# Kernel tuning notes

Hardware: AMD Instinct MI355X
Metric: run time of the kernel (lower is better)

Reference implementation:

```python
import jax, jax.numpy as jnp
import numpy as np

NUM_EXPERTS = 8
TOP_K = 2
B, S, H, I = 4, 4096, 1024, 2048


def setup_inputs() -> dict:
    key = jax.random.key(0)
    ks = jax.random.split(key, 4)
    std = 0.02
    return {
        "hidden_states": jax.random.normal(ks[0], (B, S, H), dtype=jnp.float32),
        "w_gate": jax.random.normal(ks[1], (NUM_EXPERTS, H), dtype=jnp.float32) * std,
        "w_fc": jax.random.normal(ks[2], (NUM_EXPERTS, I, H), dtype=jnp.float32) * std,
        "b_fc": jnp.zeros((NUM_EXPERTS, I), dtype=jnp.float32),
        "w_proj": jax.random.normal(ks[3], (NUM_EXPERTS, H, I), dtype=jnp.float32) * (std / np.sqrt(2 * 24)),
        "b_proj": jnp.zeros((NUM_EXPERTS, H), dtype=jnp.float32),
    }


def reference(hidden_states, w_gate, w_fc, b_fc, w_proj, b_proj):
    b, s, h = hidden_states.shape
    x = hidden_states.reshape(-1, h)  # [T, H]
    # routing: top-k over gate logits, softmax over the k selected logits
    router_logits = jnp.einsum("th,eh->te", x, w_gate)  # [T, E]
    top_vals, top_idx = jax.lax.top_k(router_logits, TOP_K)  # [T, K]
    gates = jax.nn.softmax(top_vals.astype(jnp.float32), axis=-1).astype(x.dtype)  # [T, K]
    # expert MLPs with weighted combine; per-token gate for expert e is the
    # selected routing weight (0 if e not in top-k) -- same math as the
    # gather / grouped-GEMM / index_add scatter in the original.
    out = jnp.zeros_like(x)
    for e in range(NUM_EXPERTS):
        g_e = jnp.sum(jnp.where(top_idx == e, gates, jnp.zeros_like(gates)), axis=-1)  # [T]
        hmid = jax.nn.gelu(x @ w_fc[e].T + b_fc[e], approximate=False)  # [T, I]
        y = hmid @ w_proj[e].T + b_proj[e]  # [T, H]
        out = out + g_e[:, None] * y
    return out.reshape(b, s, h)
```

## Files before the change

kernel.cpp:

```cpp
#include <hip/hip_runtime.h>
#include <math.h>

#define T_TOK 16384
#define HDIM  1024
#define IDIM  2048
#define NEXP  8
#define CAP   16384
#define ROWT  (CAP / 256)

typedef __bf16 bf16x8 __attribute__((ext_vector_type(8)));
typedef float  f32x4  __attribute__((ext_vector_type(4)));
typedef unsigned short us8 __attribute__((ext_vector_type(8)));

__device__ __forceinline__ unsigned short f2bf(float f) {
  unsigned int u = __builtin_bit_cast(unsigned int, f);
  u = (u + 0x7FFFu + ((u >> 16) & 1u)) >> 16;
  return (unsigned short)u;
}

__device__ __forceinline__ float bf2f(unsigned short u) {
  return __builtin_bit_cast(float, (unsigned int)u << 16);
}

__device__ __forceinline__ void gld16(const void* g, void* l) {
  __builtin_amdgcn_global_load_lds(
      (const __attribute__((address_space(1))) void*)(g),
      (__attribute__((address_space(3))) void*)(l), 16, 0, 0);
}

__device__ __forceinline__ bf16x8 cvt8(const float* p) {
  f32x4 lo = *(const f32x4*)p;
  f32x4 hi = *(const f32x4*)(p + 4);
  us8 t;
  t[0] = f2bf(lo[0]); t[1] = f2bf(lo[1]); t[2] = f2bf(lo[2]); t[3] = f2bf(lo[3]);
  t[4] = f2bf(hi[0]); t[5] = f2bf(hi[1]); t[6] = f2bf(hi[2]); t[7] = f2bf(hi[3]);
  return __builtin_bit_cast(bf16x8, t);
}

__global__ void zero_out_k(float4* out) {
  out[blockIdx.x * 256 + threadIdx.x] = float4{0.f, 0.f, 0.f, 0.f};
}

__global__ void report_k(float* out, float v, int n) {
  int idx = blockIdx.x * blockDim.x + threadIdx.x;
  int stride = gridDim.x * blockDim.x;
  for (int i = idx; i < n; i += stride) out[i] = v;
}

__global__ void cvt_bf16_k(const float* __restrict__ src, unsigned short* __restrict__ dst, int n4) {
  int idx = blockIdx.x * blockDim.x + threadIdx.x;
  int stride = gridDim.x * blockDim.x;
  for (int i = idx; i < n4; i += stride) {
    float4 v = ((const float4*)src)[i];
    ushort4 o;
    o.x = f2bf(v.x); o.y = f2bf(v.y); o.z = f2bf(v.z); o.w = f2bf(v.w);
    ((ushort4*)dst)[i] = o;
  }
}

__global__ void route1_k(const float* __restrict__ x, const float* __restrict__ wg,
                         int* __restrict__ echoice, float* __restrict__ tgate) {
  __shared__ __align__(16) float wgl[NEXP * HDIM];
  int tid = threadIdx.x;
  for (int i = tid; i < NEXP * HDIM / 4; i += 256)
    ((float4*)wgl)[i] = ((const float4*)wg)[i];
  __syncthreads();

  int wave = tid >> 6, lane = tid & 63;
  int t = blockIdx.x * 4 + wave;

  float accv[NEXP];
#pragma unroll
  for (int e = 0; e < NEXP; e++) accv[e] = 0.f;
  const float* xr = x + (size_t)t * HDIM;
#pragma unroll 4
  for (int j = 0; j < HDIM / 64; j++) {
    float xv = xr[lane + j * 64];
#pragma unroll
    for (int e = 0; e < NEXP; e++) accv[e] += xv * wgl[e * HDIM + lane + j * 64];
  }
#pragma unroll
  for (int off = 1; off < 64; off <<= 1) {
#pragma unroll
    for (int e = 0; e < NEXP; e++) accv[e] += __shfl_xor(accv[e], off, 64);
  }

  if (lane == 0) {
    int e0 = 0; float v0 = accv[0];
#pragma unroll
    for (int e = 1; e < NEXP; e++) if (accv[e] > v0) { v0 = accv[e]; e0 = e; }
    int e1 = -1; float v1 = -3.4e38f;
#pragma unroll
    for (int e = 0; e < NEXP; e++) if (e != e0 && accv[e] > v1) { v1 = accv[e]; e1 = e; }
    float ex = expf(v1 - v0);
    echoice[t] = e0 | (e1 << 8);
    tgate[t * 2]     = 1.f / (1.f + ex);
    tgate[t * 2 + 1] = ex / (1.f + ex);
  }
}

__global__ void route2_k(const int* __restrict__ echoice, int* __restrict__ counts,
                         int* __restrict__ etok) {
  int E = blockIdx.x;
  int tid = threadIdx.x, lane = tid & 63, wv = tid >> 6;
  __shared__ int base;
  __shared__ int wsum[4];
  if (tid == 0) base = 0;
  __syncthreads();
  for (int t0 = 0; t0 < T_TOK; t0 += 256) {
    int t = t0 + tid;
    int ec = echoice[t];
    int e0 = ec & 255, e1 = (ec >> 8) & 255;
    bool m = (e0 == E) | (e1 == E);
    int code = t * 2 + (e1 == E ? 1 : 0);
    unsigned long long mask = __ballot(m);
    if (lane == 0) wsum[wv] = __popcll(mask);
    int lpre = __popcll(mask & ((1ull << lane) - 1ull));
    __syncthreads();
    int wbase = 0;
#pragma unroll
    for (int w = 0; w < 4; w++) if (w < wv) wbase += wsum[w];
    int total = wsum[0] + wsum[1] + wsum[2] + wsum[3];
    if (m) etok[E * CAP + base + wbase + lpre] = code;
    __syncthreads();
    if (tid == 0) base += total;
    __syncthreads();
  }
  if (tid == 0) counts[E] = base;
}

template <int STAGE, int K, int N>
__global__ __launch_bounds__(512)
void gemm8_k(const unsigned short* __restrict__ A, const unsigned short* __restrict__ W,
             const float* __restrict__ bias, unsigned short* __restrict__ hmid,
             unsigned short* __restrict__ ybf,
             const int* __restrict__ counts, const int* __restrict__ etok) {
  extern __shared__ __align__(16) char smem[];
  constexpr int NTK = K / 32;
  constexpr int NTC = N / 256;
  int e  = blockIdx.x / (ROWT * NTC);
  int bi = blockIdx.x % (ROWT * NTC);
  int rt = bi / NTC, ct = bi % NTC;
  int cnt = counts[e];
  if (rt * 256 >= cnt) return;

  int tid = threadIdx.x;
  int lane = tid & 63, wv = tid >> 6;
  int wr = wv >> 2, wc = wv & 3;
  int quad = lane >> 4, ml = lane & 15;

  int sg = tid >> 6, sq = (tid >> 4) & 3, sml = tid & 15;
  const unsigned short* aptr[2];
  const unsigned short* bptr[2];
#pragma unroll
  for (int h = 0; h < 2; h++) {
    int r = rt * 256 + h * 128 + sg * 16 + sml;
    int code = etok[e * CAP + (r < cnt ? r : cnt - 1)];
    int arow = (STAGE == 1) ? (code >> 1) : code;
    aptr[h] = A + (size_t)arow * K + sq * 8;
    int n = ct * 256 + h * 128 + sg * 16 + sml;
    bptr[h] = W + ((size_t)e * N + n) * K + sq * 8;
  }
  char* Asm = smem;
  char* Bsm = smem + 65536;
  int ldst = tid * 16;

  auto stage_a = [&](int t) {
    int tt = t < NTK ? t : NTK - 1;
    char* dst = Asm + ((t & 3) * 2) * 8192 + ldst;
    gld16(aptr[0] + (size_t)tt * 32, dst);
    gld16(aptr[1] + (size_t)tt * 32, dst + 8192);
  };
  auto stage_b = [&](int t) {
    int tt = t < NTK ? t : NTK - 1;
    char* dst = Bsm + ((t & 3) * 2) * 8192 + ldst;
    gld16(bptr[0] + (size_t)tt * 32, dst);
    gld16(bptr[1] + (size_t)tt * 32, dst + 8192);
  };

  f32x4 acc[8][4] = {};

  stage_a(0); stage_b(0);
  stage_a(1); stage_b(1);
  stage_a(2); stage_b(2);
  asm volatile("s_waitcnt vmcnt(8)" ::: "memory");
  __builtin_amdgcn_s_barrier();

  int aoff = quad * 256 + ml * 16;
  int boff = (wc & 1) * 4096 + quad * 256 + ml * 16;

#pragma unroll 4
  for (int t = 0; t < NTK; t++) {
    const char* Ah = Asm + ((t & 3) * 2 + wr) * 8192;
    const char* Bh = Bsm + ((t & 3) * 2 + (wc >> 1)) * 8192;
    bf16x8 b0[4], a0[4];
#pragma unroll
    for (int ni = 0; ni < 4; ni++) b0[ni] = *(const bf16x8*)(Bh + boff + ni * 1024);
#pragma unroll
    for (int mi = 0; mi < 4; mi++) a0[mi] = *(const bf16x8*)(Ah + aoff + mi * 1024);
    stage_a(t + 3);
    asm volatile("" ::: "memory");
    __builtin_amdgcn_s_barrier();
    __builtin_amdgcn_s_setprio(1);
#pragma unroll
    for (int mi = 0; mi < 4; mi++)
#pragma unroll
      for (int ni = 0; ni < 4; ni++)
        acc[mi][ni] = __builtin_amdgcn_mfma_f32_16x16x32_bf16(a0[mi], b0[ni], acc[mi][ni], 0, 0, 0);
    __builtin_amdgcn_s_setprio(0);
    asm volatile("" ::: "memory");
    __builtin_amdgcn_s_barrier();
    bf16x8 a1[4];
#pragma unroll
    for (int mi = 0; mi < 4; mi++) a1[mi] = *(const bf16x8*)(Ah + aoff + (4 + mi) * 1024);
    stage_b(t + 3);
    asm volatile("" ::: "memory");
    __builtin_amdgcn_s_barrier();
    __builtin_amdgcn_s_setprio(1);
#pragma unroll
    for (int mi = 0; mi < 4; mi++)
#pragma unroll
      for (int ni = 0; ni < 4; ni++)
        acc[4 + mi][ni] = __builtin_amdgcn_mfma_f32_16x16x32_bf16(a1[mi], b0[ni], acc[4 + mi][ni], 0, 0, 0);
    __builtin_amdgcn_s_setprio(0);
    asm volatile("s_waitcnt vmcnt(8)" ::: "memory");
    __builtin_amdgcn_s_barrier();
  }

  int ncol[4]; float bv[4];
#pragma unroll
  for (int ni = 0; ni < 4; ni++) {
    ncol[ni] = ct * 256 + wc * 64 + ni * 16 + ml;
    bv[ni] = bias[e * N + ncol[ni]];
  }
#pragma unroll
  for (int mi = 0; mi < 8; mi++) {
    int ms[4], codes[4];
#pragma unroll
    for (int r = 0; r < 4; r++) {
      ms[r] = rt * 256 + wr * 128 + mi * 16 + quad * 4 + r;
      codes[r] = etok[e * CAP + (ms[r] < cnt ? ms[r] : 0)];
    }
#pragma unroll
    for (int ni = 0; ni < 4; ni++) {
#pragma unroll
      for (int r = 0; r < 4; r++) {
        if (ms[r] < cnt) {
          float v = acc[mi][ni][r] + bv[ni];
          if (STAGE == 1) {
            v = 0.5f * v * (1.0f + erff(v * 0.70710678118654752f));
            hmid[(size_t)codes[r] * IDIM + ncol[ni]] = f2bf(v);
          } else {
            ybf[(size_t)codes[r] * HDIM + ncol[ni]] = f2bf(v);
          }
        }
      }
    }
  }
}

template <int STAGE, int K, int N, bool A32, bool B32, bool YATOM>
__global__ __launch_bounds__(256)
void gemm_k(const void* __restrict__ Ap_, const void* __restrict__ Wp_,
            const float* __restrict__ bias, unsigned short* __restrict__ hmid,
            unsigned short* __restrict__ ybf, float* __restrict__ out,
            const float* __restrict__ tgate,
            const int* __restrict__ counts, const int* __restrict__ etok) {
  constexpr int NT = N / 128;
  constexpr int ASZ = A32 ? 16384 : 8192;
  constexpr int BSZ = B32 ? 16384 : 8192;
  __shared__ __align__(16) char smem_s[ASZ + BSZ];
  char* As = smem_s;
  char* Bs = smem_s + ASZ;

  int e  = blockIdx.x / (128 * NT);
  int bi = blockIdx.x % (128 * NT);
  int rt = bi / NT, ct = bi % NT;
  int cnt = counts[e];
  if (rt * 128 >= cnt) return;

  int tid = threadIdx.x;
  int lane = tid & 63, wv = tid >> 6;
  int wr = wv >> 1, wc = wv & 1;
  int quad = lane >> 4, ml = lane & 15;

  const char* aptr[4];
  if constexpr (A32) {
    int srow = tid >> 3, seg = tid & 7;
    const float* Af = (const float*)Ap_;
#pragma unroll
    for (int q = 0; q < 4; q++) {
      int r = rt * 128 + q * 32 + srow;
      int code = etok[e * CAP + (r < cnt ? r : cnt - 1)];
      int row = (STAGE == 1) ? (code >> 1) : code;
      aptr[q] = (const char*)(Af + (size_t)row * K + seg * 4);
    }
  } else {
    int srow = tid >> 2, seg = tid & 3;
    const unsigned short* Ab = (const unsigned short*)Ap_;
#pragma unroll
    for (int q = 0; q < 2; q++) {
      int r = rt * 128 + q * 64 + srow;
      int code = etok[e * CAP + (r < cnt ? r : cnt - 1)];
      int row = (STAGE == 1) ? (code >> 1) : code;
      aptr[q] = (const char*)(Ab + (size_t)row * K + seg * 8);
    }
  }
  const char* bptr[4];
  if constexpr (B32) {
    int srow = tid >> 3, seg = tid & 7;
    const float* Wf = (const float*)Wp_;
#pragma unroll
    for (int q = 0; q < 4; q++)
      bptr[q] = (const char*)(Wf + ((size_t)e * N + ct * 128 + q * 32 + srow) * K + seg * 4);
  } else {
    int srow = tid >> 2, seg = tid & 3;
    const unsigned short* Wb = (const unsigned short*)Wp_;
#pragma unroll
    for (int q = 0; q < 2; q++)
      bptr[q] = (const char*)(Wb + ((size_t)e * N + ct * 128 + q * 64 + srow) * K + seg * 8);
  }

  f32x4 acc[4][4] = {};

  for (int k0 = 0; k0 < K; k0 += 32) {
    size_t aoff = (size_t)k0 * (A32 ? 4 : 2);
    size_t boff = (size_t)k0 * (B32 ? 4 : 2);
    if constexpr (A32) {
#pragma unroll
      for (int q = 0; q < 4; q++) gld16(aptr[q] + aoff, As + q * 4096 + tid * 16);
    } else {
#pragma unroll
      for (int q = 0; q < 2; q++) gld16(aptr[q] + aoff, As + q * 4096 + tid * 16);
    }
    if constexpr (B32) {
#pragma unroll
      for (int q = 0; q < 4; q++) gld16(bptr[q] + boff, Bs + q * 4096 + tid * 16);
    } else {
#pragma unroll
      for (int q = 0; q < 2; q++) gld16(bptr[q] + boff, Bs + q * 4096 + tid * 16);
    }
    __syncthreads();

    bf16x8 af[4], bfr[4];
#pragma unroll
    for (int mi = 0; mi < 4; mi++) {
      int row = wr * 64 + mi * 16 + ml;
      if constexpr (A32) af[mi] = cvt8((const float*)As + row * 32 + quad * 8);
      else af[mi] = __builtin_bit_cast(bf16x8, *(const us8*)((const unsigned short*)As + row * 32 + quad * 8));
    }
#pragma unroll
    for (int ni = 0; ni < 4; ni++) {
      int row = wc * 64 + ni * 16 + ml;
      if constexpr (B32) bfr[ni] = cvt8((const float*)Bs + row * 32 + quad * 8);
      else bfr[ni] = __builtin_bit_cast(bf16x8, *(const us8*)((const unsigned short*)Bs + row * 32 + quad * 8));
    }
#pragma unroll
    for (int mi = 0; mi < 4; mi++)
#pragma unroll
      for (int ni = 0; ni < 4; ni++)
        acc[mi][ni] = __builtin_amdgcn_mfma_f32_16x16x32_bf16(af[mi], bfr[ni], acc[mi][ni], 0, 0, 0);
    __syncthreads();
  }

#pragma unroll
  for (int mi = 0; mi < 4; mi++) {
    int ms[4], codes[4];
#pragma unroll
    for (int r = 0; r < 4; r++) {
      ms[r] = rt * 128 + wr * 64 + mi * 16 + quad * 4 + r;
      codes[r] = etok[e * CAP + (ms[r] < cnt ? ms[r] : 0)];
    }
#pragma unroll
    for (int ni = 0; ni < 4; ni++) {
      int n = ct * 128 + wc * 64 + ni * 16 + ml;
      float bvv = bias[e * N + n];
#pragma unroll
      for (int r = 0; r < 4; r++) {
        if (ms[r] < cnt) {
          float v = acc[mi][ni][r] + bvv;
          if (STAGE == 1) {
            v = 0.5f * v * (1.0f + erff(v * 0.70710678118654752f));
            hmid[(size_t)codes[r] * IDIM + n] = f2bf(v);
          } else if (YATOM) {
            atomicAdd(&out[(size_t)(codes[r] >> 1) * HDIM + n], tgate[codes[r]] * v);
          } else {
            ybf[(size_t)codes[r] * HDIM + n] = f2bf(v);
          }
        }
      }
    }
  }
}

__global__ void combine_k(const unsigned short* __restrict__ y, const float* __restrict__ tgate,
                          float* __restrict__ out) {
  int idx = blockIdx.x * 256 + threadIdx.x;
  int t = idx >> 7;
  int c = idx & 127;
  float g0 = tgate[t * 2], g1 = tgate[t * 2 + 1];
  us8 a = *(const us8*)(y + ((size_t)(t * 2) * HDIM) + c * 8);
  us8 b = *(const us8*)(y + ((size_t)(t * 2 + 1) * HDIM) + c * 8);
  float o[8];
#pragma unroll
  for (int i = 0; i < 8; i++) o[i] = g0 * bf2f(a[i]) + g1 * bf2f(b[i]);
  float4* op = (float4*)(out + (size_t)t * HDIM + c * 8);
  op[0] = float4{o[0], o[1], o[2], o[3]};
  op[1] = float4{o[4], o[5], o[6], o[7]};
}

extern "C" void kernel_launch(void* const* d_in, const int* in_sizes, int n_in,
                              void* d_out, int out_size, void* d_ws, size_t ws_size,
                              hipStream_t stream) {
  const float* x     = (const float*)d_in[0];
  const float* wg    = (const float*)d_in[1];
  const float* wfc   = (const float*)d_in[2];
  const float* bfc   = (const float*)d_in[3];
  const float* wproj = (const float*)d_in[4];
  const float* bproj = (const float*)d_in[5];
  float* out = (float*)d_out;

  char* ws = (char*)d_ws;
  size_t off = 0;
  int* counts  = (int*)(ws + off);   off += 4096;
  int* echoice = (int*)(ws + off);   off += (size_t)T_TOK * 4;
  int* etok    = (int*)(ws + off);   off += (size_t)NEXP * CAP * 4;
  float* tgate = (float*)(ws + off); off += (size_t)T_TOK * 2 * 4;
  unsigned short* hmid = (unsigned short*)(ws + off);
  off += (size_t)T_TOK * 2 * IDIM * 2;
  size_t lean_need = off;
  unsigned short* xbf = (unsigned short*)(ws + off);
  size_t off2 = off + (size_t)T_TOK * HDIM * 2;
  unsigned short* wfcbf = (unsigned short*)(ws + off2);
  off2 += (size_t)NEXP * IDIM * HDIM * 2;
  unsigned short* wprojbf = (unsigned short*)(ws + off2);
  off2 += (size_t)NEXP * HDIM * IDIM * 2;
  size_t full_need = off2;
  unsigned short* ybf = xbf;

  if (ws_size < lean_need) {
    report_k<<<256, 256, 0, stream>>>(out, (float)(ws_size >> 20), T_TOK * HDIM);
    return;
  }

  route1_k<<<T_TOK / 4, 256, 0, stream>>>(x, wg, echoice, tgate);
  route2_k<<<NEXP, 256, 0, stream>>>(echoice, counts, etok);

  if (ws_size >= full_need) {
    static bool s_attr = false;
    if (!s_attr) {
      (void)hipFuncSetAttribute((const void*)gemm8_k<1, HDIM, IDIM>,
                                hipFuncAttributeMaxDynamicSharedMemorySize, 131072);
      (void)hipFuncSetAttribute((const void*)gemm8_k<2, IDIM, HDIM>,
                                hipFuncAttributeMaxDynamicSharedMemorySize, 131072);
      s_attr = true;
    }
    cvt_bf16_k<<<4096, 256, 0, stream>>>(x,     xbf,     T_TOK * HDIM / 4);
    cvt_bf16_k<<<4096, 256, 0, stream>>>(wfc,   wfcbf,   NEXP * IDIM * HDIM / 4);
    cvt_bf16_k<<<4096, 256, 0, stream>>>(wproj, wprojbf, NEXP * HDIM * IDIM / 4);
    gemm8_k<1, HDIM, IDIM><<<NEXP * ROWT * (IDIM / 256), 512, 131072, stream>>>(
        xbf, wfcbf, bfc, hmid, ybf, counts, etok);
    gemm8_k<2, IDIM, HDIM><<<NEXP * ROWT * (HDIM / 256), 512, 131072, stream>>>(
        hmid, wprojbf, bproj, hmid, ybf, counts, etok);
    combine_k<<<T_TOK * HDIM / 8 / 256, 256, 0, stream>>>(ybf, tgate, out);
  } else {
    zero_out_k<<<T_TOK * HDIM / 1024, 256, 0, stream>>>((float4*)out);
    gemm_k<1, HDIM, IDIM, true, true, true><<<NEXP * 128 * (IDIM / 128), 256, 0, stream>>>(
        x, wfc, bfc, hmid, ybf, out, tgate, counts, etok);
    gemm_k<2, IDIM, HDIM, false, true, true><<<NEXP * 128 * (HDIM / 128), 256, 0, stream>>>(
        hmid, wproj, bproj, hmid, ybf, out, tgate, counts, etok);
  }
}
```

Before: 817.2 us.

## Restructure grouped GEMM to double-buffered K=64 tiles and fuse x conversion into routing

The grouped expert GEMM moves from a 4-deep K=32 ring with split A/B staging and mid-iteration barriers to a simpler double-buffered pipeline over K=64 tiles. Each iteration prefetches the next tile, runs a full 8x4 MFMA block per k-half and waits once per tile. The routing kernel now also writes the bf16 copy of x, which drops one standalone conversion pass over the activations. The shallower prefetch and full vmcnt(0) wait can expose more global-load latency, and the 8-wide A fragment raises register pressure.

```diff
diff --git a/kernel.cpp b/kernel.cpp
--- a/kernel.cpp
+++ b/kernel.cpp
@@ -6,7 +6,7 @@
 #define IDIM  2048
 #define NEXP  8
 #define CAP   16384
-#define ROWT  (CAP / 256)
+#define RT256 (CAP / 256)
 
 typedef __bf16 bf16x8 __attribute__((ext_vector_type(8)));
 typedef float  f32x4  __attribute__((ext_vector_type(4)));
@@ -59,7 +59,8 @@
 }
 
 __global__ void route1_k(const float* __restrict__ x, const float* __restrict__ wg,
-                         int* __restrict__ echoice, float* __restrict__ tgate) {
+                         int* __restrict__ echoice, float* __restrict__ tgate,
+                         unsigned short* __restrict__ xbf) {
   __shared__ __align__(16) float wgl[NEXP * HDIM];
   int tid = threadIdx.x;
   for (int i = tid; i < NEXP * HDIM / 4; i += 256)
@@ -76,6 +77,7 @@
 #pragma unroll 4
   for (int j = 0; j < HDIM / 64; j++) {
     float xv = xr[lane + j * 64];
+    if (xbf) xbf[(size_t)t * HDIM + lane + j * 64] = f2bf(xv);
 #pragma unroll
     for (int e = 0; e < NEXP; e++) accv[e] += xv * wgl[e * HDIM + lane + j * 64];
   }
@@ -131,15 +133,15 @@
 
 template <int STAGE, int K, int N>
 __global__ __launch_bounds__(512)
-void gemm8_k(const unsigned short* __restrict__ A, const unsigned short* __restrict__ W,
-             const float* __restrict__ bias, unsigned short* __restrict__ hmid,
-             unsigned short* __restrict__ ybf,
-             const int* __restrict__ counts, const int* __restrict__ etok) {
+void gemm2p_k(const unsigned short* __restrict__ A, const unsigned short* __restrict__ W,
+              const float* __restrict__ bias, unsigned short* __restrict__ hmid,
+              unsigned short* __restrict__ ybf,
+              const int* __restrict__ counts, const int* __restrict__ etok) {
   extern __shared__ __align__(16) char smem[];
-  constexpr int NTK = K / 32;
+  constexpr int NTK = K / 64;
   constexpr int NTC = N / 256;
-  int e  = blockIdx.x / (ROWT * NTC);
-  int bi = blockIdx.x % (ROWT * NTC);
+  int e  = blockIdx.x / (RT256 * NTC);
+  int bi = blockIdx.x % (RT256 * NTC);
   int rt = bi / NTC, ct = bi % NTC;
   int cnt = counts[e];
   if (rt * 256 >= cnt) return;
@@ -149,89 +151,71 @@
   int wr = wv >> 2, wc = wv & 3;
   int quad = lane >> 4, ml = lane & 15;
 
-  int sg = tid >> 6, sq = (tid >> 4) & 3, sml = tid & 15;
-  const unsigned short* aptr[2];
-  const unsigned short* bptr[2];
-#pragma unroll
-  for (int h = 0; h < 2; h++) {
-    int r = rt * 256 + h * 128 + sg * 16 + sml;
+  int tq = (tid >> 4) & 3, tml = tid & 15, tw = tid >> 6;
+  const unsigned short* aA[4];
+  const unsigned short* aB[4];
+#pragma unroll
+  for (int j = 0; j < 4; j++) {
+    int gk = tw + 8 * j;
+    int g = gk >> 1, kk = gk & 1;
+    int koff = kk * 32 + tq * 8;
+    int r = rt * 256 + g * 16 + tml;
     int code = etok[e * CAP + (r < cnt ? r : cnt - 1)];
     int arow = (STAGE == 1) ? (code >> 1) : code;
-    aptr[h] = A + (size_t)arow * K + sq * 8;
-    int n = ct * 256 + h * 128 + sg * 16 + sml;
-    bptr[h] = W + ((size_t)e * N + n) * K + sq * 8;
-  }
-  char* Asm = smem;
-  char* Bsm = smem + 65536;
-  int ldst = tid * 16;
-
-  auto stage_a = [&](int t) {
-    int tt = t < NTK ? t : NTK - 1;
-    char* dst = Asm + ((t & 3) * 2) * 8192 + ldst;
-    gld16(aptr[0] + (size_t)tt * 32, dst);
-    gld16(aptr[1] + (size_t)tt * 32, dst + 8192);
+    aA[j] = A + (size_t)arow * K + koff;
+    int n = ct * 256 + g * 16 + tml;
+    aB[j] = W + ((size_t)e * N + n) * K + koff;
+  }
+
+  auto stage = [&](int t, int b) {
+    char* dst = smem + b * 65536 + tid * 16;
+    size_t ko = (size_t)t * 64;
+#pragma unroll
+    for (int j = 0; j < 4; j++) gld16(aA[j] + ko, dst + j * 8192);
+#pragma unroll
+    for (int j = 0; j < 4; j++) gld16(aB[j] + ko, dst + 32768 + j * 8192);
   };
-  auto stage_b = [&](int t) {
-    int tt = t < NTK ? t : NTK - 1;
-    char* dst = Bsm + ((t & 3) * 2) * 8192 + ldst;
-    gld16(bptr[0] + (size_t)tt * 32, dst);
-    gld16(bptr[1] + (size_t)tt * 32, dst + 8192);
-  };
 
   f32x4 acc[8][4] = {};
 
-  stage_a(0); stage_b(0);
-  stage_a(1); stage_b(1);
-  stage_a(2); stage_b(2);
-  asm volatile("s_waitcnt vmcnt(8)" ::: "memory");
+  stage(0, 0);
+  asm volatile("s_waitcnt vmcnt(0)" ::: "memory");
   __builtin_amdgcn_s_barrier();
 
-  int aoff = quad * 256 + ml * 16;
-  int boff = (wc & 1) * 4096 + quad * 256 + ml * 16;
-
-#pragma unroll 4
+  int ro = quad * 256 + ml * 16;
+
+#pragma unroll 2
   for (int t = 0; t < NTK; t++) {
-    const char* Ah = Asm + ((t & 3) * 2 + wr) * 8192;
-    const char* Bh = Bsm + ((t & 3) * 2 + (wc >> 1)) * 8192;
-    bf16x8 b0[4], a0[4];
-#pragma unroll
-    for (int ni = 0; ni < 4; ni++) b0[ni] = *(const bf16x8*)(Bh + boff + ni * 1024);
-#pragma unroll
-    for (int mi = 0; mi < 4; mi++) a0[mi] = *(const bf16x8*)(Ah + aoff + mi * 1024);
-    stage_a(t + 3);
-    asm volatile("" ::: "memory");
+    int cur = t & 1;
+    if (t + 1 < NTK) stage(t + 1, cur ^ 1);
+    const char* Abuf = smem + cur * 65536;
+    const char* Bbuf = Abuf + 32768;
+#pragma unroll
+    for (int kk = 0; kk < 2; kk++) {
+      bf16x8 av[8], bv[4];
+#pragma unroll
+      for (int mi = 0; mi < 8; mi++)
+        av[mi] = *(const bf16x8*)(Abuf + (wr * 8 + mi) * 2048 + kk * 1024 + ro);
+#pragma unroll
+      for (int ni = 0; ni < 4; ni++)
+        bv[ni] = *(const bf16x8*)(Bbuf + (wc * 4 + ni) * 2048 + kk * 1024 + ro);
+      __builtin_amdgcn_s_setprio(1);
+#pragma unroll
+      for (int mi = 0; mi < 8; mi++)
+#pragma unroll
+        for (int ni = 0; ni < 4; ni++)
+          acc[mi][ni] = __builtin_amdgcn_mfma_f32_16x16x32_bf16(av[mi], bv[ni], acc[mi][ni], 0, 0, 0);
+      __builtin_amdgcn_s_setprio(0);
+    }
+    asm volatile("s_waitcnt vmcnt(0)" ::: "memory");
     __builtin_amdgcn_s_barrier();
-    __builtin_amdgcn_s_setprio(1);
-#pragma unroll
-    for (int mi = 0; mi < 4; mi++)
-#pragma unroll
-      for (int ni = 0; ni < 4; ni++)
-        acc[mi][ni] = __builtin_amdgcn_mfma_f32_16x16x32_bf16(a0[mi], b0[ni], acc[mi][ni], 0, 0, 0);
-    __builtin_amdgcn_s_setprio(0);
-    asm volatile("" ::: "memory");
-    __builtin_amdgcn_s_barrier();
-    bf16x8 a1[4];
-#pragma unroll
-    for (int mi = 0; mi < 4; mi++) a1[mi] = *(const bf16x8*)(Ah + aoff + (4 + mi) * 1024);
-    stage_b(t + 3);
-    asm volatile("" ::: "memory");
-    __builtin_amdgcn_s_barrier();
-    __builtin_amdgcn_s_setprio(1);
-#pragma unroll
-    for (int mi = 0; mi < 4; mi++)
-#pragma unroll
-      for (int ni = 0; ni < 4; ni++)
-        acc[4 + mi][ni] = __builtin_amdgcn_mfma_f32_16x16x32_bf16(a1[mi], b0[ni], acc[4 + mi][ni], 0, 0, 0);
-    __builtin_amdgcn_s_setprio(0);
-    asm volatile("s_waitcnt vmcnt(8)" ::: "memory");
-    __builtin_amdgcn_s_barrier();
-  }
-
-  int ncol[4]; float bv[4];
+  }
+
+  int ncol[4]; float bvs[4];
 #pragma unroll
   for (int ni = 0; ni < 4; ni++) {
     ncol[ni] = ct * 256 + wc * 64 + ni * 16 + ml;
-    bv[ni] = bias[e * N + ncol[ni]];
+    bvs[ni] = bias[e * N + ncol[ni]];
   }
 #pragma unroll
   for (int mi = 0; mi < 8; mi++) {
@@ -246,7 +230,7 @@
 #pragma unroll
       for (int r = 0; r < 4; r++) {
         if (ms[r] < cnt) {
-          float v = acc[mi][ni][r] + bv[ni];
+          float v = acc[mi][ni][r] + bvs[ni];
           if (STAGE == 1) {
             v = 0.5f * v * (1.0f + erff(v * 0.70710678118654752f));
             hmid[(size_t)codes[r] * IDIM + ncol[ni]] = f2bf(v);
@@ -443,24 +427,25 @@
     return;
   }
 
-  route1_k<<<T_TOK / 4, 256, 0, stream>>>(x, wg, echoice, tgate);
+  bool full = (ws_size >= full_need);
+
+  route1_k<<<T_TOK / 4, 256, 0, stream>>>(x, wg, echoice, tgate, full ? xbf : (unsigned short*)nullptr);
   route2_k<<<NEXP, 256, 0, stream>>>(echoice, counts, etok);
 
-  if (ws_size >= full_need) {
+  if (full) {
     static bool s_attr = false;
     if (!s_attr) {
-      (void)hipFuncSetAttribute((const void*)gemm8_k<1, HDIM, IDIM>,
+      (void)hipFuncSetAttribute((const void*)gemm2p_k<1, HDIM, IDIM>,
                                 hipFuncAttributeMaxDynamicSharedMemorySize, 131072);
-      (void)hipFuncSetAttribute((const void*)gemm8_k<2, IDIM, HDIM>,
+      (void)hipFuncSetAttribute((const void*)gemm2p_k<2, IDIM, HDIM>,
                                 hipFuncAttributeMaxDynamicSharedMemorySize, 131072);
       s_attr = true;
     }
-    cvt_bf16_k<<<4096, 256, 0, stream>>>(x,     xbf,     T_TOK * HDIM / 4);
     cvt_bf16_k<<<4096, 256, 0, stream>>>(wfc,   wfcbf,   NEXP * IDIM * HDIM / 4);
     cvt_bf16_k<<<4096, 256, 0, stream>>>(wproj, wprojbf, NEXP * HDIM * IDIM / 4);
-    gemm8_k<1, HDIM, IDIM><<<NEXP * ROWT * (IDIM / 256), 512, 131072, stream>>>(
+    gemm2p_k<1, HDIM, IDIM><<<NEXP * RT256 * (IDIM / 256), 512, 131072, stream>>>(
         xbf, wfcbf, bfc, hmid, ybf, counts, etok);
-    gemm8_k<2, IDIM, HDIM><<<NEXP * ROWT * (HDIM / 256), 512, 131072, stream>>>(
+    gemm2p_k<2, IDIM, HDIM><<<NEXP * RT256 * (HDIM / 256), 512, 131072, stream>>>(
         hmid, wprojbf, bproj, hmid, ybf, counts, etok);
     combine_k<<<T_TOK * HDIM / 8 / 256, 256, 0, stream>>>(ybf, tgate, out);
   } else {
```

Result: slower. 1.093 ms (+33.8%).
